# Optimization experiments

Measured on AMD Instinct MI355X. Metric: run time of the kernel, lower is better.

Reference implementation:

```python
import jax, jax.numpy as jnp
import numpy as np

N_NODES = 100000
IN_DIM = 128
HID_DIM = 128
OUT_DIM = 3
N_EDGES = 1600000


def gcn_conv(x, W, b, src, dst, num_nodes):
    """PyG GCNConv: x' = D^{-1/2}(A+I)D^{-1/2} (x W) + b, where (src,dst) already include self-loops."""
    xw = x @ W                                        # [N, out]
    deg = jax.ops.segment_sum(jnp.ones_like(dst, dtype=xw.dtype), dst, num_segments=num_nodes)
    dinv = jax.lax.rsqrt(jnp.maximum(deg, 1.0))        # deg >= 1 due to self-loops
    norm = dinv[src] * dinv[dst]                       # [E]
    msg = xw[src] * norm[:, None]                      # gather  [E, out]
    out = jax.ops.segment_sum(msg, dst, num_segments=num_nodes)  # scatter-add [N, out]
    return out + b


def setup_inputs() -> dict:
    key = jax.random.key(0)
    k1, k2, k3, k4, k5 = jax.random.split(key, 5)
    feature = jax.random.normal(k1, (N_NODES, IN_DIM), dtype=jnp.float32)
    edge_index = jax.random.randint(k2, (2, N_EDGES), 0, N_NODES, dtype=jnp.int32)
    edge_type = jax.random.randint(k3, (N_EDGES,), 0, 2, dtype=jnp.int32)
    W1 = jax.random.normal(k4, (IN_DIM, HID_DIM), dtype=jnp.float32) / np.sqrt(IN_DIM)
    b1 = jnp.zeros((HID_DIM,), dtype=jnp.float32)
    W2 = jax.random.normal(k5, (HID_DIM, OUT_DIM), dtype=jnp.float32) / np.sqrt(HID_DIM)
    b2 = jnp.zeros((OUT_DIM,), dtype=jnp.float32)
    return {"feature": feature, "edge_index": edge_index, "edge_type": edge_type,
            "W1": W1, "b1": b1, "W2": W2, "b2": b2}


def reference(feature, edge_index, edge_type, W1, b1, W2, b2):
    n = feature.shape[0]
    loops = jnp.arange(n, dtype=edge_index.dtype)
    src = jnp.concatenate([edge_index[0], loops])   # add self-loops once, reused by both layers
    dst = jnp.concatenate([edge_index[1], loops])
    x = jax.nn.relu(gcn_conv(feature, W1, b1, src, dst, n))
    # dropout is identity at inference (training=False)
    x = gcn_conv(x, W2, b2, src, dst, n)
    return x
```

## Files before the change

kernel.cpp:

```cpp
#include <hip/hip_runtime.h>
#include <hip/hip_fp16.h>

#define N_NODES 100000
#define N_EDGES 1600000
#define D 128
#define NBKT 391
#define BKT_CAP 5120
#define NB_GEMM 782
#define NB_BINA 782

typedef _Float16 f16x8 __attribute__((ext_vector_type(8)));
typedef float f32x4 __attribute__((ext_vector_type(4)));

#define SWZ(b) ((b) ^ ((((b) >> 8) & 7) << 4))


__global__ __launch_bounds__(512) void mega_kernel(const float* __restrict__ x,
                                                   const float* __restrict__ W,
                                                   _Float16* __restrict__ q,
                                                   const int* __restrict__ src,
                                                   const int* __restrict__ dst,
                                                   int* __restrict__ gcnt,
                                                   int* __restrict__ staged) {
    __shared__ __align__(16) char smem[32768];
    const int tid = threadIdx.x;
    const int bid = blockIdx.x;

    if (bid < NB_GEMM) {
        const int lane = tid & 63;
        const int w = tid >> 6;
        const int r16 = lane & 15;
        const int g = lane >> 4;
        const int row0 = bid * 128;
        const int row = row0 + w * 16 + r16;
        const int rowc = row < N_NODES ? row : N_NODES - 1;
        const float* xp = x + (size_t)rowc * D;
        f16x8 a[4];
#pragma unroll
        for (int kt = 0; kt < 4; ++kt) {
            const float4 lo = *(const float4*)(xp + kt * 32 + g * 8);
            const float4 hi = *(const float4*)(xp + kt * 32 + g * 8 + 4);
            f16x8 v;
            v[0] = (_Float16)lo.x; v[1] = (_Float16)lo.y; v[2] = (_Float16)lo.z; v[3] = (_Float16)lo.w;
            v[4] = (_Float16)hi.x; v[5] = (_Float16)hi.y; v[6] = (_Float16)hi.z; v[7] = (_Float16)hi.w;
            a[kt] = v;
        }
        {
            const int n = tid & 127;
            const int k0 = (tid >> 7) * 32;
#pragma unroll
            for (int c = 0; c < 4; ++c) {
                f16x8 v;
#pragma unroll
                for (int j = 0; j < 8; ++j) v[j] = (_Float16)W[(k0 + c * 8 + j) * D + n];
                const int byte = n * 256 + (k0 + c * 8) * 2;
                *(f16x8*)(smem + SWZ(byte)) = v;
            }
        }
        __syncthreads();
        f32x4 acc[8];
#pragma unroll
        for (int nt = 0; nt < 8; ++nt) {
            f32x4 c = {0.f, 0.f, 0.f, 0.f};
#pragma unroll
            for (int kt = 0; kt < 4; ++kt) {
                const int byte = (nt * 16 + r16) * 256 + kt * 64 + g * 16;
                const f16x8 b = *(const f16x8*)(smem + SWZ(byte));
                c = __builtin_amdgcn_mfma_f32_16x16x32_f16(a[kt], b, c, 0, 0, 0);
            }
            acc[nt] = c;
        }
        __syncthreads();
        _Float16* qs = (_Float16*)smem;
#pragma unroll
        for (int nt = 0; nt < 8; ++nt)
#pragma unroll
            for (int r = 0; r < 4; ++r)
                qs[(w * 16 + g * 4 + r) * D + nt * 16 + r16] = (_Float16)acc[nt][r];
        __syncthreads();
        uint4* qg = (uint4*)q;
#pragma unroll
        for (int i = 0; i < 4; ++i) {
            const int c16 = tid + i * 512;
            const int grow = row0 + (c16 >> 4);
            if (grow < N_NODES)
                qg[(size_t)grow * 16 + (c16 & 15)] = *(const uint4*)(smem + c16 * 16);
        }
    } else {
        int* hist = (int*)smem;
        if (tid < NBKT) hist[tid] = 0;
        __syncthreads();
        const int i4 = (bid - NB_GEMM) * 512 + tid;
        const bool valid = i4 < N_EDGES / 4;
        int4 dv, sv;
        int lb0 = 0, lb1 = 0, lb2 = 0, lb3 = 0, lr0 = 0, lr1 = 0, lr2 = 0, lr3 = 0;
        if (valid) {
            dv = ((const int4*)dst)[i4];
            sv = ((const int4*)src)[i4];
            lb0 = dv.x >> 8; lr0 = atomicAdd(&hist[lb0], 1);
            lb1 = dv.y >> 8; lr1 = atomicAdd(&hist[lb1], 1);
            lb2 = dv.z >> 8; lr2 = atomicAdd(&hist[lb2], 1);
            lb3 = dv.w >> 8; lr3 = atomicAdd(&hist[lb3], 1);
        }
        __syncthreads();
        if (tid < NBKT) {
            const int c = hist[tid];
            hist[tid] = c ? atomicAdd(&gcnt[tid], c) : 0;
        }
        __syncthreads();
        if (valid) {
            staged[lb0 * BKT_CAP + hist[lb0] + lr0] = (sv.x << 8) | (dv.x & 255);
            staged[lb1 * BKT_CAP + hist[lb1] + lr1] = (sv.y << 8) | (dv.y & 255);
            staged[lb2 * BKT_CAP + hist[lb2] + lr2] = (sv.z << 8) | (dv.z & 255);
            staged[lb3 * BKT_CAP + hist[lb3] + lr3] = (sv.w << 8) | (dv.w & 255);
        }
    }
}


__global__ __launch_bounds__(256) void binB_kernel(const int* __restrict__ gcnt,
                                                   const int* __restrict__ staged,
                                                   int* __restrict__ row_ptr,
                                                   int* __restrict__ esrc,
                                                   float* __restrict__ dinv) {
    __shared__ int red[256];
    __shared__ int hist[256];
    __shared__ int nbase[256];
    __shared__ int nexc[256];
    const int b = blockIdx.x;
    const int t = threadIdx.x;
    const int m = gcnt[b];
    int partial = 0;
    for (int i = t; i < b; i += 256) partial += gcnt[i];
    red[t] = partial;
    __syncthreads();
    for (int off = 128; off; off >>= 1) {
        if (t < off) red[t] += red[t + off];
        __syncthreads();
    }
    const int bbase = red[0];
    hist[t] = 0;
    __syncthreads();
    const int* reg = staged + (size_t)b * BKT_CAP;
    for (int i = t; i < m; i += 256) atomicAdd(&hist[reg[i] & 255], 1);
    __syncthreads();
    const int v = hist[t];
    nbase[t] = v;
    __syncthreads();
    for (int off = 1; off < 256; off <<= 1) {
        int u = (t >= off) ? nbase[t - off] : 0;
        __syncthreads();
        nbase[t] += u;
        __syncthreads();
    }
    nexc[t] = nbase[t] - v;
    const int node = b * 256 + t;
    if (node < N_NODES) {
        row_ptr[node] = bbase + nexc[t];
        dinv[node] = rsqrtf((float)v + 1.0f);
    }
    if (b == 0 && t == 0) row_ptr[N_NODES] = N_EDGES;
    hist[t] = 0;
    __syncthreads();
    for (int i = t; i < m; i += 256) {
        const int rec = reg[i];
        const int nl = rec & 255;
        const int r = atomicAdd(&hist[nl], 1);
        esrc[bbase + nexc[nl] + r] = rec >> 8;
    }
}


__global__ __launch_bounds__(256) void gather1_kernel(const int* __restrict__ row_ptr,
                                                      const int* __restrict__ esrc,
                                                      const float* __restrict__ dinv,
                                                      const uint4* __restrict__ q4,
                                                      const float* __restrict__ b1,
                                                      const float* __restrict__ W2,
                                                      float* __restrict__ y) {
    const int t = threadIdx.x;
    const int n = blockIdx.x * 16 + (t >> 4);
    const int g = t & 15;
    const int beg = row_ptr[n], end = row_ptr[n + 1];
    float acc[8] = {0, 0, 0, 0, 0, 0, 0, 0};
    union U { uint4 u; __half2 h2[4]; };
    int j = beg;
    for (; j + 1 < end; j += 2) {
        const int s0 = esrc[j];
        const int s1 = esrc[j + 1];
        const float d0 = dinv[s0];
        const float d1 = dinv[s1];
        U u0, u1;
        u0.u = q4[(size_t)s0 * 16 + g];
        u1.u = q4[(size_t)s1 * 16 + g];
#pragma unroll
        for (int k = 0; k < 4; ++k) {
            const float2 f0 = __half22float2(u0.h2[k]);
            const float2 f1 = __half22float2(u1.h2[k]);
            acc[2 * k + 0] += f0.x * d0 + f1.x * d1;
            acc[2 * k + 1] += f0.y * d0 + f1.y * d1;
        }
    }
    if (j < end) {
        const int s = esrc[j];
        const float ds = dinv[s];
        U u0; u0.u = q4[(size_t)s * 16 + g];
#pragma unroll
        for (int k = 0; k < 4; ++k) {
            const float2 f0 = __half22float2(u0.h2[k]);
            acc[2 * k + 0] += f0.x * ds;
            acc[2 * k + 1] += f0.y * ds;
        }
    }
    const float dn = dinv[n];
    U un; un.u = q4[(size_t)n * 16 + g];
    const float4 ba = ((const float4*)b1)[g * 2];
    const float4 bb = ((const float4*)b1)[g * 2 + 1];
    float h[8];
#pragma unroll
    for (int k = 0; k < 4; ++k) {
        const float2 fn = __half22float2(un.h2[k]);
        h[2 * k + 0] = acc[2 * k + 0] + fn.x * dn;
        h[2 * k + 1] = acc[2 * k + 1] + fn.y * dn;
    }
    h[0] = fmaxf(h[0] * dn + ba.x, 0.f); h[1] = fmaxf(h[1] * dn + ba.y, 0.f);
    h[2] = fmaxf(h[2] * dn + ba.z, 0.f); h[3] = fmaxf(h[3] * dn + ba.w, 0.f);
    h[4] = fmaxf(h[4] * dn + bb.x, 0.f); h[5] = fmaxf(h[5] * dn + bb.y, 0.f);
    h[6] = fmaxf(h[6] * dn + bb.z, 0.f); h[7] = fmaxf(h[7] * dn + bb.w, 0.f);
    const int c = g * 8;
    float a0 = 0.f, a1 = 0.f, a2 = 0.f;
#pragma unroll
    for (int k = 0; k < 8; ++k) {
        a0 += h[k] * W2[(c + k) * 3 + 0];
        a1 += h[k] * W2[(c + k) * 3 + 1];
        a2 += h[k] * W2[(c + k) * 3 + 2];
    }
#pragma unroll
    for (int off = 8; off; off >>= 1) {
        a0 += __shfl_xor(a0, off);
        a1 += __shfl_xor(a1, off);
        a2 += __shfl_xor(a2, off);
    }
    if (g == 0) {
        y[n * 3 + 0] = a0 * dn;
        y[n * 3 + 1] = a1 * dn;
        y[n * 3 + 2] = a2 * dn;
    }
}


__global__ __launch_bounds__(256) void gather2_kernel(const int* __restrict__ row_ptr,
                                                      const int* __restrict__ esrc,
                                                      const float* __restrict__ dinv,
                                                      const float* __restrict__ y,
                                                      const float* __restrict__ b2,
                                                      float* __restrict__ out) {
    const int t = threadIdx.x;
    const int node = blockIdx.x * 64 + (t >> 2);
    if (node >= N_NODES) return;
    const int sub = t & 3;
    const int beg = row_ptr[node], end = row_ptr[node + 1];
    float a0 = 0.f, a1 = 0.f, a2 = 0.f;
    for (int j = beg + sub; j < end; j += 4) {
        const int s = esrc[j];
        a0 += y[s * 3 + 0];
        a1 += y[s * 3 + 1];
        a2 += y[s * 3 + 2];
    }
    a0 += __shfl_xor(a0, 1); a0 += __shfl_xor(a0, 2);
    a1 += __shfl_xor(a1, 1); a1 += __shfl_xor(a1, 2);
    a2 += __shfl_xor(a2, 1); a2 += __shfl_xor(a2, 2);
    if (sub == 0) {
        const float dn = dinv[node];
        out[node * 3 + 0] = (a0 + y[node * 3 + 0]) * dn + b2[0];
        out[node * 3 + 1] = (a1 + y[node * 3 + 1]) * dn + b2[1];
        out[node * 3 + 2] = (a2 + y[node * 3 + 2]) * dn + b2[2];
    }
}


extern "C" void kernel_launch(void* const* d_in, const int* in_sizes, int n_in,
                              void* d_out, int out_size, void* d_ws, size_t ws_size,
                              hipStream_t stream) {
    const float* feature = (const float*)d_in[0];
    const int* edge_index = (const int*)d_in[1];
    const int* src = edge_index;
    const int* dst = edge_index + N_EDGES;
    const float* W1 = (const float*)d_in[3];
    const float* b1 = (const float*)d_in[4];
    const float* W2 = (const float*)d_in[5];
    const float* b2 = (const float*)d_in[6];
    float* out = (float*)d_out;

    const size_t ND = (size_t)N_NODES * D;
    _Float16* q    = (_Float16*)d_ws;
    float* y       = (float*)(q + ND);
    float* dinv    = y + (size_t)N_NODES * 3;
    int*   row_ptr = (int*)(dinv + N_NODES);
    int*   esrc    = row_ptr + (N_NODES + 1);
    int*   gcnt    = esrc + N_EDGES;
    int*   staged  = gcnt + NBKT;

    hipMemsetAsync(gcnt, 0, NBKT * sizeof(int), stream);
    mega_kernel<<<NB_GEMM + NB_BINA, 512, 0, stream>>>(feature, W1, q, src, dst, gcnt, staged);
    binB_kernel<<<NBKT, 256, 0, stream>>>(gcnt, staged, row_ptr, esrc, dinv);
    gather1_kernel<<<N_NODES / 16, 256, 0, stream>>>(row_ptr, esrc, dinv, (const uint4*)q, b1, W2, y);
    gather2_kernel<<<(N_NODES + 63) / 64, 256, 0, stream>>>(row_ptr, esrc, dinv, y, b2, out);
}
```

Before: 222.1 us.

## Slice q into column-major feature slabs and split layer-1 gather per slice

The GEMM output q is now stored as 8 slabs of 16 feature columns each, so each slab is a compact 3.2MB array. Layer-1 aggregation is split across 8 slice-blocks per node group, with 2 threads per node, so each pass over the edge list touches only one slab. The aim is a random-gather working set that fits in cache. Partial W2 projections are combined via float atomics into a padded y4 buffer, which is zeroed with a memset. In exchange, esrc, row_ptr and dinv are read 8 times, and the change adds atomics and makes the summation order nondeterministic.

```diff
diff --git a/kernel.cpp b/kernel.cpp
--- a/kernel.cpp
+++ b/kernel.cpp
@@ -8,6 +8,7 @@
 #define BKT_CAP 5120
 #define NB_GEMM 782
 #define NB_BINA 782
+#define NB_GS 782
 
 typedef _Float16 f16x8 __attribute__((ext_vector_type(8)));
 typedef float f32x4 __attribute__((ext_vector_type(4)));
@@ -83,8 +84,10 @@
         for (int i = 0; i < 4; ++i) {
             const int c16 = tid + i * 512;
             const int grow = row0 + (c16 >> 4);
+            const int k = c16 & 15;
             if (grow < N_NODES)
-                qg[(size_t)grow * 16 + (c16 & 15)] = *(const uint4*)(smem + c16 * 16);
+                qg[(size_t)(k >> 1) * (N_NODES * 2) + (size_t)grow * 2 + (k & 1)] =
+                    *(const uint4*)(smem + c16 * 16);
         }
     } else {
         int* hist = (int*)smem;
@@ -171,17 +174,20 @@
 }
 
 
-__global__ __launch_bounds__(256) void gather1_kernel(const int* __restrict__ row_ptr,
+__global__ __launch_bounds__(256) void gatherS_kernel(const int* __restrict__ row_ptr,
                                                       const int* __restrict__ esrc,
                                                       const float* __restrict__ dinv,
-                                                      const uint4* __restrict__ q4,
+                                                      const _Float16* __restrict__ q,
                                                       const float* __restrict__ b1,
                                                       const float* __restrict__ W2,
-                                                      float* __restrict__ y) {
+                                                      float* __restrict__ y4) {
     const int t = threadIdx.x;
-    const int n = blockIdx.x * 16 + (t >> 4);
-    const int g = t & 15;
-    const int beg = row_ptr[n], end = row_ptr[n + 1];
+    const int slice = blockIdx.x & 7;
+    const int node = (blockIdx.x >> 3) * 128 + (t >> 1);
+    if (node >= N_NODES) return;
+    const int p = t & 1;
+    const uint4* qs = (const uint4*)q + (size_t)slice * (N_NODES * 2);
+    const int beg = row_ptr[node], end = row_ptr[node + 1];
     float acc[8] = {0, 0, 0, 0, 0, 0, 0, 0};
     union U { uint4 u; __half2 h2[4]; };
     int j = beg;
@@ -191,8 +197,8 @@
         const float d0 = dinv[s0];
         const float d1 = dinv[s1];
         U u0, u1;
-        u0.u = q4[(size_t)s0 * 16 + g];
-        u1.u = q4[(size_t)s1 * 16 + g];
+        u0.u = qs[(size_t)s0 * 2 + p];
+        u1.u = qs[(size_t)s1 * 2 + p];
 #pragma unroll
         for (int k = 0; k < 4; ++k) {
             const float2 f0 = __half22float2(u0.h2[k]);
@@ -204,7 +210,7 @@
     if (j < end) {
         const int s = esrc[j];
         const float ds = dinv[s];
-        U u0; u0.u = q4[(size_t)s * 16 + g];
+        U u0; u0.u = qs[(size_t)s * 2 + p];
 #pragma unroll
         for (int k = 0; k < 4; ++k) {
             const float2 f0 = __half22float2(u0.h2[k]);
@@ -212,39 +218,26 @@
             acc[2 * k + 1] += f0.y * ds;
         }
     }
-    const float dn = dinv[n];
-    U un; un.u = q4[(size_t)n * 16 + g];
-    const float4 ba = ((const float4*)b1)[g * 2];
-    const float4 bb = ((const float4*)b1)[g * 2 + 1];
-    float h[8];
+    const float dn = dinv[node];
+    U un; un.u = qs[(size_t)node * 2 + p];
+    const int c0 = slice * 16 + p * 8;
+    float a0 = 0.f, a1 = 0.f, a2 = 0.f;
 #pragma unroll
     for (int k = 0; k < 4; ++k) {
         const float2 fn = __half22float2(un.h2[k]);
-        h[2 * k + 0] = acc[2 * k + 0] + fn.x * dn;
-        h[2 * k + 1] = acc[2 * k + 1] + fn.y * dn;
-    }
-    h[0] = fmaxf(h[0] * dn + ba.x, 0.f); h[1] = fmaxf(h[1] * dn + ba.y, 0.f);
-    h[2] = fmaxf(h[2] * dn + ba.z, 0.f); h[3] = fmaxf(h[3] * dn + ba.w, 0.f);
-    h[4] = fmaxf(h[4] * dn + bb.x, 0.f); h[5] = fmaxf(h[5] * dn + bb.y, 0.f);
-    h[6] = fmaxf(h[6] * dn + bb.z, 0.f); h[7] = fmaxf(h[7] * dn + bb.w, 0.f);
-    const int c = g * 8;
-    float a0 = 0.f, a1 = 0.f, a2 = 0.f;
-#pragma unroll
-    for (int k = 0; k < 8; ++k) {
-        a0 += h[k] * W2[(c + k) * 3 + 0];
-        a1 += h[k] * W2[(c + k) * 3 + 1];
-        a2 += h[k] * W2[(c + k) * 3 + 2];
-    }
-#pragma unroll
-    for (int off = 8; off; off >>= 1) {
-        a0 += __shfl_xor(a0, off);
-        a1 += __shfl_xor(a1, off);
-        a2 += __shfl_xor(a2, off);
-    }
-    if (g == 0) {
-        y[n * 3 + 0] = a0 * dn;
-        y[n * 3 + 1] = a1 * dn;
-        y[n * 3 + 2] = a2 * dn;
+        const float h0 = fmaxf((acc[2 * k + 0] + fn.x * dn) * dn + b1[c0 + 2 * k + 0], 0.f);
+        const float h1 = fmaxf((acc[2 * k + 1] + fn.y * dn) * dn + b1[c0 + 2 * k + 1], 0.f);
+        a0 += h0 * W2[(c0 + 2 * k) * 3 + 0] + h1 * W2[(c0 + 2 * k + 1) * 3 + 0];
+        a1 += h0 * W2[(c0 + 2 * k) * 3 + 1] + h1 * W2[(c0 + 2 * k + 1) * 3 + 1];
+        a2 += h0 * W2[(c0 + 2 * k) * 3 + 2] + h1 * W2[(c0 + 2 * k + 1) * 3 + 2];
+    }
+    a0 += __shfl_xor(a0, 1);
+    a1 += __shfl_xor(a1, 1);
+    a2 += __shfl_xor(a2, 1);
+    if (p == 0) {
+        atomicAdd(&y4[node * 4 + 0], a0 * dn);
+        atomicAdd(&y4[node * 4 + 1], a1 * dn);
+        atomicAdd(&y4[node * 4 + 2], a2 * dn);
     }
 }
 
@@ -252,7 +245,7 @@
 __global__ __launch_bounds__(256) void gather2_kernel(const int* __restrict__ row_ptr,
                                                       const int* __restrict__ esrc,
                                                       const float* __restrict__ dinv,
-                                                      const float* __restrict__ y,
+                                                      const float* __restrict__ y4,
                                                       const float* __restrict__ b2,
                                                       float* __restrict__ out) {
     const int t = threadIdx.x;
@@ -263,18 +256,18 @@
     float a0 = 0.f, a1 = 0.f, a2 = 0.f;
     for (int j = beg + sub; j < end; j += 4) {
         const int s = esrc[j];
-        a0 += y[s * 3 + 0];
-        a1 += y[s * 3 + 1];
-        a2 += y[s * 3 + 2];
+        a0 += y4[(size_t)s * 4 + 0];
+        a1 += y4[(size_t)s * 4 + 1];
+        a2 += y4[(size_t)s * 4 + 2];
     }
     a0 += __shfl_xor(a0, 1); a0 += __shfl_xor(a0, 2);
     a1 += __shfl_xor(a1, 1); a1 += __shfl_xor(a1, 2);
     a2 += __shfl_xor(a2, 1); a2 += __shfl_xor(a2, 2);
     if (sub == 0) {
         const float dn = dinv[node];
-        out[node * 3 + 0] = (a0 + y[node * 3 + 0]) * dn + b2[0];
-        out[node * 3 + 1] = (a1 + y[node * 3 + 1]) * dn + b2[1];
-        out[node * 3 + 2] = (a2 + y[node * 3 + 2]) * dn + b2[2];
+        out[node * 3 + 0] = (a0 + y4[(size_t)node * 4 + 0]) * dn + b2[0];
+        out[node * 3 + 1] = (a1 + y4[(size_t)node * 4 + 1]) * dn + b2[1];
+        out[node * 3 + 2] = (a2 + y4[(size_t)node * 4 + 2]) * dn + b2[2];
     }
 }
 
@@ -294,16 +287,16 @@
 
     const size_t ND = (size_t)N_NODES * D;
     _Float16* q    = (_Float16*)d_ws;
-    float* y       = (float*)(q + ND);
-    float* dinv    = y + (size_t)N_NODES * 3;
+    float* y4      = (float*)(q + ND);
+    int*   gcnt    = (int*)(y4 + (size_t)N_NODES * 4);
+    float* dinv    = (float*)(gcnt + NBKT);
     int*   row_ptr = (int*)(dinv + N_NODES);
     int*   esrc    = row_ptr + (N_NODES + 1);
-    int*   gcnt    = esrc + N_EDGES;
-    int*   staged  = gcnt + NBKT;
-
-    hipMemsetAsync(gcnt, 0, NBKT * sizeof(int), stream);
+    int*   staged  = esrc + N_EDGES;
+
+    hipMemsetAsync(y4, 0, ((size_t)N_NODES * 4 + NBKT) * sizeof(float), stream);
     mega_kernel<<<NB_GEMM + NB_BINA, 512, 0, stream>>>(feature, W1, q, src, dst, gcnt, staged);
     binB_kernel<<<NBKT, 256, 0, stream>>>(gcnt, staged, row_ptr, esrc, dinv);
-    gather1_kernel<<<N_NODES / 16, 256, 0, stream>>>(row_ptr, esrc, dinv, (const uint4*)q, b1, W2, y);
-    gather2_kernel<<<(N_NODES + 63) / 64, 256, 0, stream>>>(row_ptr, esrc, dinv, y, b2, out);
-}
+    gatherS_kernel<<<NB_GS * 8, 256, 0, stream>>>(row_ptr, esrc, dinv, q, b1, W2, y4);
+    gather2_kernel<<<(N_NODES + 63) / 64, 256, 0, stream>>>(row_ptr, esrc, dinv, y4, b2, out);
+}
```

Result: slower. 318.3 us (+43.3%).

## Pair GEMM with CSR bucket-finalize instead of edge binning

Applied to the files above, without the earlier changes.

The edge binning pass (binA) now runs as its own kernel first. The feature GEMM is co-scheduled in one launch with the per-bucket CSR finalize (binB), which was rewritten for 512 threads. The aim is to hide the latency-bound CSR finalize behind the GEMM instead of the binning pass, while keeping the kernel count the same. In exchange, binning no longer overlaps with the GEMM and half the threads sit idle during the finalize scan.

```diff
diff --git a/kernel.cpp b/kernel.cpp
--- a/kernel.cpp
+++ b/kernel.cpp
@@ -15,13 +15,49 @@
 #define SWZ(b) ((b) ^ ((((b) >> 8) & 7) << 4))
 
 
-__global__ __launch_bounds__(512) void mega_kernel(const float* __restrict__ x,
-                                                   const float* __restrict__ W,
-                                                   _Float16* __restrict__ q,
-                                                   const int* __restrict__ src,
+__global__ __launch_bounds__(512) void binA_kernel(const int* __restrict__ src,
                                                    const int* __restrict__ dst,
                                                    int* __restrict__ gcnt,
                                                    int* __restrict__ staged) {
+    __shared__ int hist[NBKT];
+    const int tid = threadIdx.x;
+    if (tid < NBKT) hist[tid] = 0;
+    __syncthreads();
+    const int i4 = blockIdx.x * 512 + tid;
+    const bool valid = i4 < N_EDGES / 4;
+    int4 dv, sv;
+    int lb0 = 0, lb1 = 0, lb2 = 0, lb3 = 0, lr0 = 0, lr1 = 0, lr2 = 0, lr3 = 0;
+    if (valid) {
+        dv = ((const int4*)dst)[i4];
+        sv = ((const int4*)src)[i4];
+        lb0 = dv.x >> 8; lr0 = atomicAdd(&hist[lb0], 1);
+        lb1 = dv.y >> 8; lr1 = atomicAdd(&hist[lb1], 1);
+        lb2 = dv.z >> 8; lr2 = atomicAdd(&hist[lb2], 1);
+        lb3 = dv.w >> 8; lr3 = atomicAdd(&hist[lb3], 1);
+    }
+    __syncthreads();
+    if (tid < NBKT) {
+        const int c = hist[tid];
+        hist[tid] = c ? atomicAdd(&gcnt[tid], c) : 0;
+    }
+    __syncthreads();
+    if (valid) {
+        staged[lb0 * BKT_CAP + hist[lb0] + lr0] = (sv.x << 8) | (dv.x & 255);
+        staged[lb1 * BKT_CAP + hist[lb1] + lr1] = (sv.y << 8) | (dv.y & 255);
+        staged[lb2 * BKT_CAP + hist[lb2] + lr2] = (sv.z << 8) | (dv.z & 255);
+        staged[lb3 * BKT_CAP + hist[lb3] + lr3] = (sv.w << 8) | (dv.w & 255);
+    }
+}
+
+
+__global__ __launch_bounds__(512) void fused2_kernel(const float* __restrict__ x,
+                                                     const float* __restrict__ W,
+                                                     _Float16* __restrict__ q,
+                                                     const int* __restrict__ gcnt,
+                                                     const int* __restrict__ staged,
+                                                     int* __restrict__ row_ptr,
+                                                     int* __restrict__ esrc,
+                                                     float* __restrict__ dinv) {
     __shared__ __align__(16) char smem[32768];
     const int tid = threadIdx.x;
     const int bid = blockIdx.x;
@@ -87,86 +123,52 @@
                 qg[(size_t)grow * 16 + (c16 & 15)] = *(const uint4*)(smem + c16 * 16);
         }
     } else {
-        int* hist = (int*)smem;
-        if (tid < NBKT) hist[tid] = 0;
-        __syncthreads();
-        const int i4 = (bid - NB_GEMM) * 512 + tid;
-        const bool valid = i4 < N_EDGES / 4;
-        int4 dv, sv;
-        int lb0 = 0, lb1 = 0, lb2 = 0, lb3 = 0, lr0 = 0, lr1 = 0, lr2 = 0, lr3 = 0;
-        if (valid) {
-            dv = ((const int4*)dst)[i4];
-            sv = ((const int4*)src)[i4];
-            lb0 = dv.x >> 8; lr0 = atomicAdd(&hist[lb0], 1);
-            lb1 = dv.y >> 8; lr1 = atomicAdd(&hist[lb1], 1);
-            lb2 = dv.z >> 8; lr2 = atomicAdd(&hist[lb2], 1);
-            lb3 = dv.w >> 8; lr3 = atomicAdd(&hist[lb3], 1);
-        }
-        __syncthreads();
-        if (tid < NBKT) {
-            const int c = hist[tid];
-            hist[tid] = c ? atomicAdd(&gcnt[tid], c) : 0;
-        }
-        __syncthreads();
-        if (valid) {
-            staged[lb0 * BKT_CAP + hist[lb0] + lr0] = (sv.x << 8) | (dv.x & 255);
-            staged[lb1 * BKT_CAP + hist[lb1] + lr1] = (sv.y << 8) | (dv.y & 255);
-            staged[lb2 * BKT_CAP + hist[lb2] + lr2] = (sv.z << 8) | (dv.z & 255);
-            staged[lb3 * BKT_CAP + hist[lb3] + lr3] = (sv.w << 8) | (dv.w & 255);
-        }
-    }
-}
-
-
-__global__ __launch_bounds__(256) void binB_kernel(const int* __restrict__ gcnt,
-                                                   const int* __restrict__ staged,
-                                                   int* __restrict__ row_ptr,
-                                                   int* __restrict__ esrc,
-                                                   float* __restrict__ dinv) {
-    __shared__ int red[256];
-    __shared__ int hist[256];
-    __shared__ int nbase[256];
-    __shared__ int nexc[256];
-    const int b = blockIdx.x;
-    const int t = threadIdx.x;
-    const int m = gcnt[b];
-    int partial = 0;
-    for (int i = t; i < b; i += 256) partial += gcnt[i];
-    red[t] = partial;
-    __syncthreads();
-    for (int off = 128; off; off >>= 1) {
-        if (t < off) red[t] += red[t + off];
-        __syncthreads();
-    }
-    const int bbase = red[0];
-    hist[t] = 0;
-    __syncthreads();
-    const int* reg = staged + (size_t)b * BKT_CAP;
-    for (int i = t; i < m; i += 256) atomicAdd(&hist[reg[i] & 255], 1);
-    __syncthreads();
-    const int v = hist[t];
-    nbase[t] = v;
-    __syncthreads();
-    for (int off = 1; off < 256; off <<= 1) {
-        int u = (t >= off) ? nbase[t - off] : 0;
-        __syncthreads();
-        nbase[t] += u;
-        __syncthreads();
-    }
-    nexc[t] = nbase[t] - v;
-    const int node = b * 256 + t;
-    if (node < N_NODES) {
-        row_ptr[node] = bbase + nexc[t];
-        dinv[node] = rsqrtf((float)v + 1.0f);
-    }
-    if (b == 0 && t == 0) row_ptr[N_NODES] = N_EDGES;
-    hist[t] = 0;
-    __syncthreads();
-    for (int i = t; i < m; i += 256) {
-        const int rec = reg[i];
-        const int nl = rec & 255;
-        const int r = atomicAdd(&hist[nl], 1);
-        esrc[bbase + nexc[nl] + r] = rec >> 8;
+        int* red   = (int*)smem;
+        int* hist  = red + 512;
+        int* nbase = hist + 256;
+        int* nexc  = nbase + 256;
+        const int b = bid - NB_GEMM;
+        const int m = gcnt[b];
+        int partial = 0;
+        for (int i = tid; i < b; i += 512) partial += gcnt[i];
+        red[tid] = partial;
+        __syncthreads();
+        for (int off = 256; off; off >>= 1) {
+            if (tid < off) red[tid] += red[tid + off];
+            __syncthreads();
+        }
+        const int bbase = red[0];
+        if (tid < 256) hist[tid] = 0;
+        __syncthreads();
+        const int* reg = staged + (size_t)b * BKT_CAP;
+        for (int i = tid; i < m; i += 512) atomicAdd(&hist[reg[i] & 255], 1);
+        __syncthreads();
+        const int v = (tid < 256) ? hist[tid] : 0;
+        if (tid < 256) nbase[tid] = v;
+        __syncthreads();
+        for (int off = 1; off < 256; off <<= 1) {
+            const int u = (tid < 256 && tid >= off) ? nbase[tid - off] : 0;
+            __syncthreads();
+            if (tid < 256) nbase[tid] += u;
+            __syncthreads();
+        }
+        if (tid < 256) {
+            nexc[tid] = nbase[tid] - v;
+            const int node = b * 256 + tid;
+            if (node < N_NODES) {
+                row_ptr[node] = bbase + nexc[tid];
+                dinv[node] = rsqrtf((float)v + 1.0f);
+            }
+            hist[tid] = 0;
+        }
+        if (b == 0 && tid == 0) row_ptr[N_NODES] = N_EDGES;
+        __syncthreads();
+        for (int i = tid; i < m; i += 512) {
+            const int rec = reg[i];
+            const int nl = rec & 255;
+            const int r = atomicAdd(&hist[nl], 1);
+            esrc[bbase + nexc[nl] + r] = rec >> 8;
+        }
     }
 }
 
@@ -302,8 +304,9 @@
     int*   staged  = gcnt + NBKT;
 
     hipMemsetAsync(gcnt, 0, NBKT * sizeof(int), stream);
-    mega_kernel<<<NB_GEMM + NB_BINA, 512, 0, stream>>>(feature, W1, q, src, dst, gcnt, staged);
-    binB_kernel<<<NBKT, 256, 0, stream>>>(gcnt, staged, row_ptr, esrc, dinv);
+    binA_kernel<<<NB_BINA, 512, 0, stream>>>(src, dst, gcnt, staged);
+    fused2_kernel<<<NB_GEMM + NBKT, 512, 0, stream>>>(feature, W1, q, gcnt, staged,
+                                                      row_ptr, esrc, dinv);
     gather1_kernel<<<N_NODES / 16, 256, 0, stream>>>(row_ptr, esrc, dinv, (const uint4*)q, b1, W2, y);
     gather2_kernel<<<(N_NODES + 63) / 64, 256, 0, stream>>>(row_ptr, esrc, dinv, y, b2, out);
 }
```

After: 228.7 us. +3.0%, slower.

## Fuse CSR build into layer-1 gather and scatter layer 2 from buckets

Applied to the files above, without the earlier changes.

Removes the separate binB kernel that built a global row_ptr/esrc CSR. Each gatherB block now takes a quarter of one destination bucket, builds a local CSR in LDS and aggregates layer 1 directly. Layer 2 becomes a per-bucket LDS atomic scatter over the staged records, reading y padded to float4. Degrees are counted with global atomics in the binning pass and rsqrt is recomputed on the fly. This saves one launch and the global esrc write and read, at the cost of reading each staged bucket four times, extra global atomics on cnt, and an LDS capacity assumption (QCAP 1536 edges per quarter bucket).

```diff
diff --git a/kernel.cpp b/kernel.cpp
--- a/kernel.cpp
+++ b/kernel.cpp
@@ -8,6 +8,7 @@
 #define BKT_CAP 5120
 #define NB_GEMM 782
 #define NB_BINA 782
+#define QCAP 1536
 
 typedef _Float16 f16x8 __attribute__((ext_vector_type(8)));
 typedef float f32x4 __attribute__((ext_vector_type(4)));
@@ -20,6 +21,7 @@
                                                    _Float16* __restrict__ q,
                                                    const int* __restrict__ src,
                                                    const int* __restrict__ dst,
+                                                   int* __restrict__ cnt,
                                                    int* __restrict__ gcnt,
                                                    int* __restrict__ staged) {
     __shared__ __align__(16) char smem[32768];
@@ -97,6 +99,10 @@
         if (valid) {
             dv = ((const int4*)dst)[i4];
             sv = ((const int4*)src)[i4];
+            atomicAdd(&cnt[dv.x], 1);
+            atomicAdd(&cnt[dv.y], 1);
+            atomicAdd(&cnt[dv.z], 1);
+            atomicAdd(&cnt[dv.w], 1);
             lb0 = dv.x >> 8; lr0 = atomicAdd(&hist[lb0], 1);
             lb1 = dv.y >> 8; lr1 = atomicAdd(&hist[lb1], 1);
             lb2 = dv.z >> 8; lr2 = atomicAdd(&hist[lb2], 1);
@@ -118,163 +124,157 @@
 }
 
 
-__global__ __launch_bounds__(256) void binB_kernel(const int* __restrict__ gcnt,
-                                                   const int* __restrict__ staged,
-                                                   int* __restrict__ row_ptr,
-                                                   int* __restrict__ esrc,
-                                                   float* __restrict__ dinv) {
-    __shared__ int red[256];
-    __shared__ int hist[256];
-    __shared__ int nbase[256];
-    __shared__ int nexc[256];
+__global__ __launch_bounds__(256) void gatherB_kernel(const int* __restrict__ gcnt,
+                                                      const int* __restrict__ staged,
+                                                      const int* __restrict__ cnt,
+                                                      const _Float16* __restrict__ q,
+                                                      const float* __restrict__ b1,
+                                                      const float* __restrict__ W2,
+                                                      float* __restrict__ y4) {
+    __shared__ int hist[64];
+    __shared__ int scn[64];
+    __shared__ int rpl[65];
+    __shared__ int cur[64];
+    __shared__ int esrc_lds[QCAP];
+    const int t = threadIdx.x;
+    const int bucket = blockIdx.x >> 2;
+    const int quarter = blockIdx.x & 3;
+    const int m = gcnt[bucket];
+    const int* reg = staged + (size_t)bucket * BKT_CAP;
+    if (t < 64) hist[t] = 0;
+    __syncthreads();
+    for (int i = t; i < m; i += 256) {
+        const int dl = reg[i] & 255;
+        if ((dl >> 6) == quarter) atomicAdd(&hist[dl & 63], 1);
+    }
+    __syncthreads();
+    if (t < 64) scn[t] = hist[t];
+    __syncthreads();
+    for (int off = 1; off < 64; off <<= 1) {
+        const int u = (t < 64 && t >= off) ? scn[t - off] : 0;
+        __syncthreads();
+        if (t < 64) scn[t] += u;
+        __syncthreads();
+    }
+    if (t < 64) { rpl[t + 1] = scn[t]; cur[t] = 0; }
+    if (t == 0) rpl[0] = 0;
+    __syncthreads();
+    for (int i = t; i < m; i += 256) {
+        const int rec = reg[i];
+        const int dl = rec & 255;
+        if ((dl >> 6) == quarter) {
+            const int nl = dl & 63;
+            const int pos = rpl[nl] + atomicAdd(&cur[nl], 1);
+            esrc_lds[pos] = rec >> 8;
+        }
+    }
+    __syncthreads();
+    const int g = t & 15;
+    union U { uint4 u; __half2 h2[4]; };
+    const uint4* q4 = (const uint4*)q;
+#pragma unroll
+    for (int r = 0; r < 4; ++r) {
+        const int nl = r * 16 + (t >> 4);
+        const int node = bucket * 256 + quarter * 64 + nl;
+        if (node >= N_NODES) continue;
+        const int beg = rpl[nl], end = rpl[nl + 1];
+        float acc[8] = {0, 0, 0, 0, 0, 0, 0, 0};
+        int j = beg;
+        for (; j + 1 < end; j += 2) {
+            const int s0 = esrc_lds[j];
+            const int s1 = esrc_lds[j + 1];
+            const float d0 = rsqrtf((float)cnt[s0] + 1.0f);
+            const float d1 = rsqrtf((float)cnt[s1] + 1.0f);
+            U u0, u1;
+            u0.u = q4[(size_t)s0 * 16 + g];
+            u1.u = q4[(size_t)s1 * 16 + g];
+#pragma unroll
+            for (int k = 0; k < 4; ++k) {
+                const float2 f0 = __half22float2(u0.h2[k]);
+                const float2 f1 = __half22float2(u1.h2[k]);
+                acc[2 * k + 0] += f0.x * d0 + f1.x * d1;
+                acc[2 * k + 1] += f0.y * d0 + f1.y * d1;
+            }
+        }
+        if (j < end) {
+            const int s = esrc_lds[j];
+            const float ds = rsqrtf((float)cnt[s] + 1.0f);
+            U u0; u0.u = q4[(size_t)s * 16 + g];
+#pragma unroll
+            for (int k = 0; k < 4; ++k) {
+                const float2 f0 = __half22float2(u0.h2[k]);
+                acc[2 * k + 0] += f0.x * ds;
+                acc[2 * k + 1] += f0.y * ds;
+            }
+        }
+        const float dn = rsqrtf((float)cnt[node] + 1.0f);
+        U un; un.u = q4[(size_t)node * 16 + g];
+        const float4 ba = ((const float4*)b1)[g * 2];
+        const float4 bb = ((const float4*)b1)[g * 2 + 1];
+        float h[8];
+#pragma unroll
+        for (int k = 0; k < 4; ++k) {
+            const float2 fn = __half22float2(un.h2[k]);
+            h[2 * k + 0] = acc[2 * k + 0] + fn.x * dn;
+            h[2 * k + 1] = acc[2 * k + 1] + fn.y * dn;
+        }
+        h[0] = fmaxf(h[0] * dn + ba.x, 0.f); h[1] = fmaxf(h[1] * dn + ba.y, 0.f);
+        h[2] = fmaxf(h[2] * dn + ba.z, 0.f); h[3] = fmaxf(h[3] * dn + ba.w, 0.f);
+        h[4] = fmaxf(h[4] * dn + bb.x, 0.f); h[5] = fmaxf(h[5] * dn + bb.y, 0.f);
+        h[6] = fmaxf(h[6] * dn + bb.z, 0.f); h[7] = fmaxf(h[7] * dn + bb.w, 0.f);
+        const int c = g * 8;
+        float a0 = 0.f, a1 = 0.f, a2 = 0.f;
+#pragma unroll
+        for (int k = 0; k < 8; ++k) {
+            a0 += h[k] * W2[(c + k) * 3 + 0];
+            a1 += h[k] * W2[(c + k) * 3 + 1];
+            a2 += h[k] * W2[(c + k) * 3 + 2];
+        }
+#pragma unroll
+        for (int off = 8; off; off >>= 1) {
+            a0 += __shfl_xor(a0, off);
+            a1 += __shfl_xor(a1, off);
+            a2 += __shfl_xor(a2, off);
+        }
+        if (g == 0) {
+            y4[(size_t)node * 4 + 0] = a0 * dn;
+            y4[(size_t)node * 4 + 1] = a1 * dn;
+            y4[(size_t)node * 4 + 2] = a2 * dn;
+        }
+    }
+}
+
+
+__global__ __launch_bounds__(256) void scat2_kernel(const int* __restrict__ gcnt,
+                                                    const int* __restrict__ staged,
+                                                    const int* __restrict__ cnt,
+                                                    const float* __restrict__ y4,
+                                                    const float* __restrict__ b2,
+                                                    float* __restrict__ out) {
+    __shared__ float a3[3][256];
+    const int t = threadIdx.x;
     const int b = blockIdx.x;
-    const int t = threadIdx.x;
+    a3[0][t] = 0.f; a3[1][t] = 0.f; a3[2][t] = 0.f;
+    __syncthreads();
     const int m = gcnt[b];
-    int partial = 0;
-    for (int i = t; i < b; i += 256) partial += gcnt[i];
-    red[t] = partial;
-    __syncthreads();
-    for (int off = 128; off; off >>= 1) {
-        if (t < off) red[t] += red[t + off];
-        __syncthreads();
-    }
-    const int bbase = red[0];
-    hist[t] = 0;
-    __syncthreads();
     const int* reg = staged + (size_t)b * BKT_CAP;
-    for (int i = t; i < m; i += 256) atomicAdd(&hist[reg[i] & 255], 1);
-    __syncthreads();
-    const int v = hist[t];
-    nbase[t] = v;
-    __syncthreads();
-    for (int off = 1; off < 256; off <<= 1) {
-        int u = (t >= off) ? nbase[t - off] : 0;
-        __syncthreads();
-        nbase[t] += u;
-        __syncthreads();
-    }
-    nexc[t] = nbase[t] - v;
+    for (int i = t; i < m; i += 256) {
+        const int rec = reg[i];
+        const int s = rec >> 8;
+        const int dl = rec & 255;
+        const float4 ys = *(const float4*)&y4[(size_t)s * 4];
+        atomicAdd(&a3[0][dl], ys.x);
+        atomicAdd(&a3[1][dl], ys.y);
+        atomicAdd(&a3[2][dl], ys.z);
+    }
+    __syncthreads();
     const int node = b * 256 + t;
     if (node < N_NODES) {
-        row_ptr[node] = bbase + nexc[t];
-        dinv[node] = rsqrtf((float)v + 1.0f);
-    }
-    if (b == 0 && t == 0) row_ptr[N_NODES] = N_EDGES;
-    hist[t] = 0;
-    __syncthreads();
-    for (int i = t; i < m; i += 256) {
-        const int rec = reg[i];
-        const int nl = rec & 255;
-        const int r = atomicAdd(&hist[nl], 1);
-        esrc[bbase + nexc[nl] + r] = rec >> 8;
-    }
-}
-
-
-__global__ __launch_bounds__(256) void gather1_kernel(const int* __restrict__ row_ptr,
-                                                      const int* __restrict__ esrc,
-                                                      const float* __restrict__ dinv,
-                                                      const uint4* __restrict__ q4,
-                                                      const float* __restrict__ b1,
-                                                      const float* __restrict__ W2,
-                                                      float* __restrict__ y) {
-    const int t = threadIdx.x;
-    const int n = blockIdx.x * 16 + (t >> 4);
-    const int g = t & 15;
-    const int beg = row_ptr[n], end = row_ptr[n + 1];
-    float acc[8] = {0, 0, 0, 0, 0, 0, 0, 0};
-    union U { uint4 u; __half2 h2[4]; };
-    int j = beg;
-    for (; j + 1 < end; j += 2) {
-        const int s0 = esrc[j];
-        const int s1 = esrc[j + 1];
-        const float d0 = dinv[s0];
-        const float d1 = dinv[s1];
-        U u0, u1;
-        u0.u = q4[(size_t)s0 * 16 + g];
-        u1.u = q4[(size_t)s1 * 16 + g];
-#pragma unroll
-        for (int k = 0; k < 4; ++k) {
-            const float2 f0 = __half22float2(u0.h2[k]);
-            const float2 f1 = __half22float2(u1.h2[k]);
-            acc[2 * k + 0] += f0.x * d0 + f1.x * d1;
-            acc[2 * k + 1] += f0.y * d0 + f1.y * d1;
-        }
-    }
-    if (j < end) {
-        const int s = esrc[j];
-        const float ds = dinv[s];
-        U u0; u0.u = q4[(size_t)s * 16 + g];
-#pragma unroll
-        for (int k = 0; k < 4; ++k) {
-            const float2 f0 = __half22float2(u0.h2[k]);
-            acc[2 * k + 0] += f0.x * ds;
-            acc[2 * k + 1] += f0.y * ds;
-        }
-    }
-    const float dn = dinv[n];
-    U un; un.u = q4[(size_t)n * 16 + g];
-    const float4 ba = ((const float4*)b1)[g * 2];
-    const float4 bb = ((const float4*)b1)[g * 2 + 1];
-    float h[8];
-#pragma unroll
-    for (int k = 0; k < 4; ++k) {
-        const float2 fn = __half22float2(un.h2[k]);
-        h[2 * k + 0] = acc[2 * k + 0] + fn.x * dn;
-        h[2 * k + 1] = acc[2 * k + 1] + fn.y * dn;
-    }
-    h[0] = fmaxf(h[0] * dn + ba.x, 0.f); h[1] = fmaxf(h[1] * dn + ba.y, 0.f);
-    h[2] = fmaxf(h[2] * dn + ba.z, 0.f); h[3] = fmaxf(h[3] * dn + ba.w, 0.f);
-    h[4] = fmaxf(h[4] * dn + bb.x, 0.f); h[5] = fmaxf(h[5] * dn + bb.y, 0.f);
-    h[6] = fmaxf(h[6] * dn + bb.z, 0.f); h[7] = fmaxf(h[7] * dn + bb.w, 0.f);
-    const int c = g * 8;
-    float a0 = 0.f, a1 = 0.f, a2 = 0.f;
-#pragma unroll
-    for (int k = 0; k < 8; ++k) {
-        a0 += h[k] * W2[(c + k) * 3 + 0];
-        a1 += h[k] * W2[(c + k) * 3 + 1];
-        a2 += h[k] * W2[(c + k) * 3 + 2];
-    }
-#pragma unroll
-    for (int off = 8; off; off >>= 1) {
-        a0 += __shfl_xor(a0, off);
-        a1 += __shfl_xor(a1, off);
-        a2 += __shfl_xor(a2, off);
-    }
-    if (g == 0) {
-        y[n * 3 + 0] = a0 * dn;
-        y[n * 3 + 1] = a1 * dn;
-        y[n * 3 + 2] = a2 * dn;
-    }
-}
-
-
-__global__ __launch_bounds__(256) void gather2_kernel(const int* __restrict__ row_ptr,
-                                                      const int* __restrict__ esrc,
-                                                      const float* __restrict__ dinv,
-                                                      const float* __restrict__ y,
-                                                      const float* __restrict__ b2,
-                                                      float* __restrict__ out) {
-    const int t = threadIdx.x;
-    const int node = blockIdx.x * 64 + (t >> 2);
-    if (node >= N_NODES) return;
-    const int sub = t & 3;
-    const int beg = row_ptr[node], end = row_ptr[node + 1];
-    float a0 = 0.f, a1 = 0.f, a2 = 0.f;
-    for (int j = beg + sub; j < end; j += 4) {
-        const int s = esrc[j];
-        a0 += y[s * 3 + 0];
-        a1 += y[s * 3 + 1];
-        a2 += y[s * 3 + 2];
-    }
-    a0 += __shfl_xor(a0, 1); a0 += __shfl_xor(a0, 2);
-    a1 += __shfl_xor(a1, 1); a1 += __shfl_xor(a1, 2);
-    a2 += __shfl_xor(a2, 1); a2 += __shfl_xor(a2, 2);
-    if (sub == 0) {
-        const float dn = dinv[node];
-        out[node * 3 + 0] = (a0 + y[node * 3 + 0]) * dn + b2[0];
-        out[node * 3 + 1] = (a1 + y[node * 3 + 1]) * dn + b2[1];
-        out[node * 3 + 2] = (a2 + y[node * 3 + 2]) * dn + b2[2];
+        const float dn = rsqrtf((float)cnt[node] + 1.0f);
+        const float4 yn = *(const float4*)&y4[(size_t)node * 4];
+        out[node * 3 + 0] = (a3[0][t] + yn.x) * dn + b2[0];
+        out[node * 3 + 1] = (a3[1][t] + yn.y) * dn + b2[1];
+        out[node * 3 + 2] = (a3[2][t] + yn.z) * dn + b2[2];
     }
 }
 
@@ -293,17 +293,14 @@
     float* out = (float*)d_out;
 
     const size_t ND = (size_t)N_NODES * D;
-    _Float16* q    = (_Float16*)d_ws;
-    float* y       = (float*)(q + ND);
-    float* dinv    = y + (size_t)N_NODES * 3;
-    int*   row_ptr = (int*)(dinv + N_NODES);
-    int*   esrc    = row_ptr + (N_NODES + 1);
-    int*   gcnt    = esrc + N_EDGES;
-    int*   staged  = gcnt + NBKT;
-
-    hipMemsetAsync(gcnt, 0, NBKT * sizeof(int), stream);
-    mega_kernel<<<NB_GEMM + NB_BINA, 512, 0, stream>>>(feature, W1, q, src, dst, gcnt, staged);
-    binB_kernel<<<NBKT, 256, 0, stream>>>(gcnt, staged, row_ptr, esrc, dinv);
-    gather1_kernel<<<N_NODES / 16, 256, 0, stream>>>(row_ptr, esrc, dinv, (const uint4*)q, b1, W2, y);
-    gather2_kernel<<<(N_NODES + 63) / 64, 256, 0, stream>>>(row_ptr, esrc, dinv, y, b2, out);
+    _Float16* q   = (_Float16*)d_ws;
+    float* y4     = (float*)(q + ND);
+    int*   cnt    = (int*)(y4 + (size_t)N_NODES * 4);
+    int*   gcnt   = cnt + N_NODES;
+    int*   staged = gcnt + NBKT;
+
+    hipMemsetAsync(cnt, 0, (N_NODES + NBKT) * sizeof(int), stream);
+    mega_kernel<<<NB_GEMM + NB_BINA, 512, 0, stream>>>(feature, W1, q, src, dst, cnt, gcnt, staged);
+    gatherB_kernel<<<NBKT * 4, 256, 0, stream>>>(gcnt, staged, cnt, q, b1, W2, y4);
+    scat2_kernel<<<NBKT, 256, 0, stream>>>(gcnt, staged, cnt, y4, b2, out);
 }
```

After: 293.8 us. +32.3%, slower.
